# Kernel optimization log

Measured on AMD Instinct MI355X. Metric: run time of the kernel, lower is better.

Reference implementation:

```python
import jax, jax.numpy as jnp
import numpy as np

EPS = 1e-7
N_NODES = 30000
N_EDGES = 300000
GNN_DIM = 256
ENC_HID = 128
OUT_DIM = 3
N_LAYERS = 4


def _glorot(key, shape):
    fan_in, fan_out = shape[-2], shape[-1]
    s = jnp.sqrt(6.0 / (fan_in + fan_out))
    return jax.random.uniform(key, shape, jnp.float32, -s, s)


def setup_inputs() -> dict:
    key = jax.random.key(0)
    ks = jax.random.split(key, 12)
    x = jax.random.normal(ks[0], (N_NODES, 1), jnp.float32)
    edge_attr = jax.random.normal(ks[1], (N_EDGES, 1), jnp.float32)
    edge_index = jax.random.randint(ks[2], (2, N_EDGES), 0, N_NODES, jnp.int64)
    return {
        "x": x,
        "edge_attr": edge_attr,
        "edge_index": edge_index,
        # node encoder MLP: 1 -> 128 -> ReLU -> 256
        "node_w1": _glorot(ks[3], (1, ENC_HID)),
        "node_b1": jnp.zeros((ENC_HID,), jnp.float32),
        "node_w2": _glorot(ks[4], (ENC_HID, GNN_DIM)),
        "node_b2": jnp.zeros((GNN_DIM,), jnp.float32),
        # edge encoder MLP: 1 -> 128 -> ReLU -> 256
        "edge_w1": _glorot(ks[5], (1, ENC_HID)),
        "edge_b1": jnp.zeros((ENC_HID,), jnp.float32),
        "edge_w2": _glorot(ks[6], (ENC_HID, GNN_DIM)),
        "edge_b2": jnp.zeros((GNN_DIM,), jnp.float32),
        # 4 GENConv layers, each internal MLP is a single Linear(256, 256)
        "gnn_w": _glorot(ks[7], (N_LAYERS, GNN_DIM, GNN_DIM)),
        "gnn_b": jnp.zeros((N_LAYERS, GNN_DIM), jnp.float32),
        # output head: Linear(256, 3)
        "out_w": _glorot(ks[8], (GNN_DIM, OUT_DIM)),
        "out_b": jnp.zeros((OUT_DIM,), jnp.float32),
    }


def reference(x, edge_attr, edge_index, node_w1, node_b1, node_w2, node_b2,
              edge_w1, edge_b1, edge_w2, edge_b2, gnn_w, gnn_b, out_w, out_b):
    n = x.shape[0]
    # encoders (MLP, no norm, ReLU between layers, plain last layer)
    h = jax.nn.relu(x @ node_w1 + node_b1) @ node_w2 + node_b2            # [N, 256]
    e = jax.nn.relu(edge_attr @ edge_w1 + edge_b1) @ edge_w2 + edge_b2    # [E, 256]
    src = edge_index[0]  # x_j (source, messages flow source -> target)
    dst = edge_index[1]  # aggregation target
    for l in range(gnn_w.shape[0]):
        # GENConv message: relu(x_j + edge_attr) + eps
        msg = jax.nn.relu(h[src] + e) + EPS                               # [E, 256]
        agg = jax.ops.segment_sum(msg, dst, num_segments=n)               # [N, 256]
        # update: mlp(aggr + x_dst); num_layers=1 -> single Linear
        h = (agg + h) @ gnn_w[l] + gnn_b[l]
    return h @ out_w + out_b                                              # [N, 3]
```

## Files before the change

kernel.cpp:

```cpp
#include <hip/hip_runtime.h>
#include <stdint.h>

#define EPS_F 1e-7f

typedef float f32x4 __attribute__((ext_vector_type(4)));
typedef float f32x8 __attribute__((ext_vector_type(8)));
typedef short short8 __attribute__((ext_vector_type(8)));
typedef unsigned short u16;
typedef unsigned short ushort4v __attribute__((ext_vector_type(4)));
typedef unsigned short ushort8v __attribute__((ext_vector_type(8)));
typedef unsigned int uint4v __attribute__((ext_vector_type(4)));

__device__ __forceinline__ short f2bf(float f) {
  unsigned u = __float_as_uint(f);
  unsigned r = u + 0x7FFFu + ((u >> 16) & 1u);
  return (short)(r >> 16);
}
__device__ __forceinline__ float bf2f(u16 u) {
  return __uint_as_float((unsigned)u << 16);
}

__global__ void build_meta_kernel(const float* __restrict__ w1, const float* __restrict__ b1,
                                  float* __restrict__ knots, int* __restrict__ jrank,
                                  int* __restrict__ act0, int* __restrict__ segsel) {
  __shared__ float s_kx[128];
  __shared__ float s_sorted[128];
  int t = threadIdx.x;
  float w = w1[t], b = b1[t];
  float kx = (w != 0.0f) ? (-b / w) : 3.4e38f;
  s_kx[t] = kx;
  int a0 = (w < 0.0f) || (w == 0.0f && b > 0.0f);
  __syncthreads();
  int r = 0;
  for (int i = 0; i < 128; ++i) {
    float o = s_kx[i];
    if (o < kx || (o == kx && i < t)) ++r;
  }
  jrank[t] = r;
  act0[t] = a0;
  knots[r] = kx;
  s_sorted[r] = kx;
  __syncthreads();
  if (t == 0 && segsel) {
    int lo = 0, hi = 128;
    while (lo < hi) { int m = (lo + hi) >> 1; if (s_sorted[m] < -1.0f) lo = m + 1; else hi = m; }
    segsel[0] = lo;
    lo = 0; hi = 128;
    while (lo < hi) { int m = (lo + hi) >> 1; if (s_sorted[m] < 1.0f) lo = m + 1; else hi = m; }
    segsel[1] = lo;
  }
}

__global__ void build_seg_kernel(const float* __restrict__ w1, const float* __restrict__ b1,
                                 const float* __restrict__ w2, const float* __restrict__ b2,
                                 const int* __restrict__ jrank, const int* __restrict__ act0,
                                 float* __restrict__ segA, float* __restrict__ segB,
                                 unsigned* __restrict__ ABpack) {
  int s = blockIdx.x;
  int t = threadIdx.x;
  __shared__ float s_w1[128], s_b1[128];
  __shared__ int s_on[128];
  if (t < 128) {
    s_w1[t] = w1[t];
    s_b1[t] = b1[t];
    s_on[t] = act0[t] ^ (jrank[t] < s ? 1 : 0);
  }
  __syncthreads();
  float A = 0.0f, B = b2[t];
#pragma unroll 4
  for (int j = 0; j < 128; ++j) {
    if (s_on[j]) {
      float w2v = w2[j * 256 + t];
      A = fmaf(s_w1[j], w2v, A);
      B = fmaf(s_b1[j], w2v, B);
    }
  }
  segA[s * 256 + t] = A;
  segB[s * 256 + t] = B;
  if (ABpack) {
    unsigned a = (unsigned)(u16)f2bf(A);
    unsigned bb = (unsigned)(u16)f2bf(B);
    ABpack[s * 256 + t] = a | (bb << 16);
  }
}

__global__ void apply_enc_kernel(const float* __restrict__ in, int nrows,
                                 const float* __restrict__ knots, const float* __restrict__ segA,
                                 const float* __restrict__ segB, u16* __restrict__ outbf) {
  __shared__ float s_kx[128];
  int t = threadIdx.x;
  if (t < 128) s_kx[t] = knots[t];
  __syncthreads();
  int r0 = blockIdx.x * 16;
  int rEnd = r0 + 16;
  if (rEnd > nrows) rEnd = nrows;
  for (int r = r0; r < rEnd; ++r) {
    float x = in[r];
    int lo = 0, hi = 128;
    while (lo < hi) { int mid = (lo + hi) >> 1; if (s_kx[mid] < x) lo = mid + 1; else hi = mid; }
    outbf[(size_t)r * 256 + t] = (u16)f2bf(fmaf(segA[lo * 256 + t], x, segB[lo * 256 + t]));
  }
}

__global__ void zero_kernel(int* __restrict__ p, int n) {
  int i = blockIdx.x * blockDim.x + threadIdx.x;
  if (i < n) p[i] = 0;
}

__global__ void hist_kernel(const int* __restrict__ dst, int E, int* __restrict__ counts) {
  int i = blockIdx.x * blockDim.x + threadIdx.x;
  if (i < E) atomicAdd(&counts[dst[i]], 1);
}

__global__ void scan_p1_kernel(const int* __restrict__ counts, int n,
                               int* __restrict__ blocksums) {
  __shared__ int tmp[256];
  int t = threadIdx.x;
  int i = blockIdx.x * 256 + t;
  tmp[t] = (i < n) ? counts[i] : 0;
  __syncthreads();
  for (int off = 128; off > 0; off >>= 1) {
    if (t < off) tmp[t] += tmp[t + off];
    __syncthreads();
  }
  if (t == 0) blocksums[blockIdx.x] = tmp[0];
}

__global__ void scan_p2_kernel(int* __restrict__ blocksums, int nb,
                               int* __restrict__ row_start, int n) {
  __shared__ int tmp[256];
  int t = threadIdx.x;
  int v = (t < nb) ? blocksums[t] : 0;
  tmp[t] = v;
  __syncthreads();
  for (int off = 1; off < 256; off <<= 1) {
    int add = (t >= off) ? tmp[t - off] : 0;
    __syncthreads();
    tmp[t] += add;
    __syncthreads();
  }
  if (t < nb) blocksums[t] = tmp[t] - v;
  if (t == 0) row_start[n] = tmp[255];
}

__global__ void scan_p3_kernel(const int* __restrict__ counts, int n,
                               const int* __restrict__ blocksums,
                               int* __restrict__ row_start) {
  __shared__ int tmp[256];
  int t = threadIdx.x;
  int i = blockIdx.x * 256 + t;
  int v = (i < n) ? counts[i] : 0;
  tmp[t] = v;
  __syncthreads();
  for (int off = 1; off < 256; off <<= 1) {
    int add = (t >= off) ? tmp[t - off] : 0;
    __syncthreads();
    tmp[t] += add;
    __syncthreads();
  }
  if (i < n) row_start[i] = blocksums[blockIdx.x] + tmp[t] - v;
}

__global__ void fill_kernel(const int* __restrict__ srcA, const int* __restrict__ dstA,
                            const float* __restrict__ eattr, int E,
                            const int* __restrict__ row_start, int* __restrict__ cursor,
                            const float* __restrict__ knotsE, int2* __restrict__ csr) {
  __shared__ float s_kx[128];
  if (threadIdx.x < 128) s_kx[threadIdx.x] = knotsE[threadIdx.x];
  __syncthreads();
  int i = blockIdx.x * blockDim.x + threadIdx.x;
  if (i >= E) return;
  int s = srcA[i], d = dstA[i];
  float x = eattr[i];
  int lo = 0, hi = 128;
  while (lo < hi) { int mid = (lo + hi) >> 1; if (s_kx[mid] < x) lo = mid + 1; else hi = mid; }
  int pos = row_start[d] + atomicAdd(&cursor[d], 1);
  csr[pos] = make_int2(s | (lo << 17), __float_as_int(x));
}

__global__ void convw_kernel(const float* __restrict__ W, short* __restrict__ WT) {
  int l = blockIdx.x >> 8, nn = blockIdx.x & 255, k = threadIdx.x;
  WT[((size_t)l * 256 + nn) * 256 + k] = f2bf(W[((size_t)l * 256 + k) * 256 + nn]);
}

#define PAIR_FETCH(k)                                                              \
  int si##k = p + 2 * (k) + half; si##k = (si##k < hi) ? si##k : hi - 1;           \
  int2 e##k = ec[si##k];                                                           \
  ushort8v hv##k = *(const ushort8v*)(hbf + (size_t)(e##k.x & 0x1FFFF) * 256 + dl);

#define PAIR_COMP(k) {                                                             \
    float mk = (p + 2 * (k) + half < hi) ? 1.0f : 0.0f;                            \
    float xk = __int_as_float(e##k.y);                                             \
    int gk = e##k.x >> 17;                                                         \
    if (__builtin_expect(__ballot(gk != segN && gk != segP) != 0ull, 0)) {         \
      uint4v ab0 = *(const uint4v*)(AB + (size_t)gk * 256 + dl);                   \
      uint4v ab1 = *(const uint4v*)(AB + (size_t)gk * 256 + dl + 4);               \
      _Pragma("unroll") for (int j = 0; j < 8; ++j) {                              \
        unsigned abj = (j < 4) ? ab0[j] : ab1[j - 4];                              \
        float Ae = __uint_as_float(abj << 16);                                     \
        float Be = __uint_as_float(abj & 0xFFFF0000u);                             \
        float tt = bf2f(hv##k[j]) + fmaf(Ae, xk, Be);                              \
        acc[j] = fmaf(mk, fmaxf(tt, 0.0f), acc[j]);                                \
      }                                                                            \
    } else {                                                                       \
      bool isN = (gk == segN);                                                     \
      _Pragma("unroll") for (int j = 0; j < 8; ++j) {                              \
        float Ae = isN ? An[j] : Ap[j];                                            \
        float Be = isN ? Bn[j] : Bp[j];                                            \
        float tt = bf2f(hv##k[j]) + fmaf(Ae, xk, Be);                              \
        acc[j] = fmaf(mk, fmaxf(tt, 0.0f), acc[j]);                                \
      }                                                                            \
    }                                                                              \
  }

__global__ __launch_bounds__(256, 2) void layer_kernel(
    const u16* __restrict__ hbf, const int2* __restrict__ csr,
    const int* __restrict__ rowSt,
    const unsigned* __restrict__ AB, const int* __restrict__ segsel,
    const short* __restrict__ WT, const float* __restrict__ bias,
    u16* __restrict__ houtbf, float* __restrict__ outp,
    const float* __restrict__ ow3, const float* __restrict__ ob3, int N) {
  __shared__ u16 As[16][264];
  __shared__ int2 ecache[4][256];
  __shared__ float sw[768];
  __shared__ float sh[4][16][3];
  int wv = threadIdx.x >> 6, lane = threadIdx.x & 63;
  int nbase = blockIdx.x * 16;
  int d0 = lane * 4;
  int v0 = nbase + wv * 4;
  int half = lane >> 5;
  int dl = (lane & 31) * 8;

  if (outp) {
    for (int i = threadIdx.x; i < 768; i += 256) sw[i] = ow3[i];
  }

  int segN = segsel[0], segP = segsel[1];
  f32x8 An, Bn, Ap, Bp;
  {
    uint4v n0 = *(const uint4v*)(AB + (size_t)segN * 256 + dl);
    uint4v n1 = *(const uint4v*)(AB + (size_t)segN * 256 + dl + 4);
    uint4v p0v = *(const uint4v*)(AB + (size_t)segP * 256 + dl);
    uint4v p1v = *(const uint4v*)(AB + (size_t)segP * 256 + dl + 4);
#pragma unroll
    for (int j = 0; j < 8; ++j) {
      unsigned nj = (j < 4) ? n0[j] : n1[j - 4];
      unsigned pj = (j < 4) ? p0v[j] : p1v[j - 4];
      An[j] = __uint_as_float(nj << 16);
      Bn[j] = __uint_as_float(nj & 0xFFFF0000u);
      Ap[j] = __uint_as_float(pj << 16);
      Bp[j] = __uint_as_float(pj & 0xFFFF0000u);
    }
  }

  int rv0 = rowSt[v0], rv1 = rowSt[v0 + 1], rv2 = rowSt[v0 + 2];
  int rv3 = rowSt[v0 + 3], rv4 = rowSt[v0 + 4];
  int range = rv4 - rv0;
  const int2* ec = &ecache[wv][0];

  if (__builtin_expect(range <= 256, 1)) {
    for (int s = lane; s < range; s += 64) ecache[wv][s] = csr[(size_t)rv0 + s];
    for (int i = 0; i < 4; ++i) {
      int v = v0 + i;
      int lo = ((i == 0) ? rv0 : (i == 1) ? rv1 : (i == 2) ? rv2 : rv3) - rv0;
      int hi = ((i == 0) ? rv1 : (i == 1) ? rv2 : (i == 2) ? rv3 : rv4) - rv0;
      int deg = hi - lo;
      ushort8v sv = *(const ushort8v*)(hbf + (size_t)v * 256 + dl);
      float de = (float)deg * EPS_F;
      f32x8 acc = {0.f, 0.f, 0.f, 0.f, 0.f, 0.f, 0.f, 0.f};
      for (int p = lo; p < hi; p += 8) {
        PAIR_FETCH(0); PAIR_FETCH(1); PAIR_FETCH(2); PAIR_FETCH(3);
        PAIR_COMP(0); PAIR_COMP(1); PAIR_COMP(2); PAIR_COMP(3);
      }
      ushort8v ob;
#pragma unroll
      for (int j = 0; j < 8; ++j) {
        float tot = acc[j] + __shfl_xor(acc[j], 32);
        ob[j] = (u16)f2bf(bf2f(sv[j]) + de + tot);
      }
      if (half == 0) *(ushort8v*)&As[wv * 4 + i][dl] = ob;
    }
  } else {
    for (int i = 0; i < 4; ++i) {
      int v = v0 + i;
      int lo = (i == 0) ? rv0 : (i == 1) ? rv1 : (i == 2) ? rv2 : rv3;
      int hi = (i == 0) ? rv1 : (i == 1) ? rv2 : (i == 2) ? rv3 : rv4;
      int deg = hi - lo;
      ushort4v sv = *(const ushort4v*)(hbf + (size_t)v * 256 + d0);
      float de = (float)deg * EPS_F;
      f32x4 acc;
      acc.x = bf2f(sv.x) + de; acc.y = bf2f(sv.y) + de;
      acc.z = bf2f(sv.z) + de; acc.w = bf2f(sv.w) + de;
      for (int p = lo; p < hi; ++p) {
        int2 e = csr[(size_t)p];
        ushort4v hv = *(const ushort4v*)(hbf + (size_t)(e.x & 0x1FFFF) * 256 + d0);
        float x = __int_as_float(e.y);
        int g = __builtin_amdgcn_readfirstlane(e.x) >> 17;
        f32x4 Ae, Be;
        uint4v ab = *(const uint4v*)(AB + (size_t)g * 256 + d0);
#pragma unroll
        for (int j = 0; j < 4; ++j) {
          Ae[j] = __uint_as_float(ab[j] << 16);
          Be[j] = __uint_as_float(ab[j] & 0xFFFF0000u);
        }
#pragma unroll
        for (int j = 0; j < 4; ++j)
          acc[j] += fmaxf(bf2f(hv[j]) + fmaf(Ae[j], x, Be[j]), 0.0f);
      }
      ushort4v ob;
      ob.x = (u16)f2bf(acc.x); ob.y = (u16)f2bf(acc.y);
      ob.z = (u16)f2bf(acc.z); ob.w = (u16)f2bf(acc.w);
      *(ushort4v*)&As[wv * 4 + i][d0] = ob;
    }
  }
  __syncthreads();

  int colb = lane & 15, rowf = lane & 15, kgrp = (lane >> 4) * 8;
  int c0 = wv * 64;
  const short* wtc = WT + (size_t)(c0 + colb) * 256;
  const u16* Ar = &As[rowf][0];
  f32x4 acc0 = {0.f, 0.f, 0.f, 0.f}, acc1 = acc0, acc2 = acc0, acc3 = acc0;
  short8 b0 = *(const short8*)(wtc + kgrp);
  short8 b1 = *(const short8*)(wtc + 4096 + kgrp);
  short8 b2 = *(const short8*)(wtc + 8192 + kgrp);
  short8 b3 = *(const short8*)(wtc + 12288 + kgrp);
#pragma unroll
  for (int kt = 0; kt < 8; ++kt) {
    int k0 = kt * 32 + kgrp;
    short8 af = *(const short8*)(Ar + k0);
    short8 n0, n1, n2, n3;
    if (kt < 7) {
      int kn = k0 + 32;
      n0 = *(const short8*)(wtc + kn);
      n1 = *(const short8*)(wtc + 4096 + kn);
      n2 = *(const short8*)(wtc + 8192 + kn);
      n3 = *(const short8*)(wtc + 12288 + kn);
    }
    acc0 = __builtin_amdgcn_mfma_f32_16x16x32_bf16(af, b0, acc0, 0, 0, 0);
    acc1 = __builtin_amdgcn_mfma_f32_16x16x32_bf16(af, b1, acc1, 0, 0, 0);
    acc2 = __builtin_amdgcn_mfma_f32_16x16x32_bf16(af, b2, acc2, 0, 0, 0);
    acc3 = __builtin_amdgcn_mfma_f32_16x16x32_bf16(af, b3, acc3, 0, 0, 0);
    if (kt < 7) { b0 = n0; b1 = n1; b2 = n2; b3 = n3; }
  }
  int rbase = (lane >> 4) * 4;
  if (houtbf) {
#pragma unroll
    for (int nbk = 0; nbk < 4; ++nbk) {
      f32x4 a = (nbk == 0) ? acc0 : (nbk == 1) ? acc1 : (nbk == 2) ? acc2 : acc3;
      int col = c0 + nbk * 16 + colb;
      float bv = bias[col];
#pragma unroll
      for (int rr = 0; rr < 4; ++rr) {
        int vv = nbase + rbase + rr;
        if (vv < N) houtbf[(size_t)vv * 256 + col] = (u16)f2bf(a[rr] + bv);
      }
    }
  }
  if (outp) {
    float p[4][3];
#pragma unroll
    for (int rr = 0; rr < 4; ++rr) {
      p[rr][0] = 0.f; p[rr][1] = 0.f; p[rr][2] = 0.f;
    }
#pragma unroll
    for (int nbk = 0; nbk < 4; ++nbk) {
      f32x4 a = (nbk == 0) ? acc0 : (nbk == 1) ? acc1 : (nbk == 2) ? acc2 : acc3;
      int col = c0 + nbk * 16 + colb;
      float bv = bias[col];
#pragma unroll
      for (int rr = 0; rr < 4; ++rr) {
        float val = a[rr] + bv;
#pragma unroll
        for (int o = 0; o < 3; ++o) p[rr][o] = fmaf(val, sw[col * 3 + o], p[rr][o]);
      }
    }
#pragma unroll
    for (int rr = 0; rr < 4; ++rr)
#pragma unroll
      for (int o = 0; o < 3; ++o) {
        float s = p[rr][o];
        s += __shfl_xor(s, 1, 16);
        s += __shfl_xor(s, 2, 16);
        s += __shfl_xor(s, 4, 16);
        s += __shfl_xor(s, 8, 16);
        if (colb == 0) sh[wv][rbase + rr][o] = s;
      }
    __syncthreads();
    int t = threadIdx.x;
    if (t < 48) {
      int row = t / 3, o = t % 3;
      float s = sh[0][row][o] + sh[1][row][o] + sh[2][row][o] + sh[3][row][o] + ob3[o];
      int vv = nbase + row;
      if (vv < N) outp[(size_t)vv * 3 + o] = s;
    }
  }
}

extern "C" void kernel_launch(void* const* d_in, const int* in_sizes, int n_in,
                              void* d_out, int out_size, void* d_ws, size_t ws_size,
                              hipStream_t stream) {
  const float* x     = (const float*)d_in[0];
  const float* eattr = (const float*)d_in[1];
  const int*   eidx  = (const int*)d_in[2];
  const float* nw1 = (const float*)d_in[3];
  const float* nb1 = (const float*)d_in[4];
  const float* nw2 = (const float*)d_in[5];
  const float* nb2 = (const float*)d_in[6];
  const float* ew1 = (const float*)d_in[7];
  const float* eb1 = (const float*)d_in[8];
  const float* ew2 = (const float*)d_in[9];
  const float* eb2 = (const float*)d_in[10];
  const float* gw  = (const float*)d_in[11];
  const float* gb  = (const float*)d_in[12];
  const float* ow  = (const float*)d_in[13];
  const float* ob  = (const float*)d_in[14];

  int N = in_sizes[0];
  int E = in_sizes[1];
  const int* srcA = eidx;
  const int* dstA = eidx + E;

  char* ws = (char*)d_ws;
  auto al = [](size_t v) { return (v + 255) & ~(size_t)255; };
  size_t off = 0;
  u16* hbfA    = (u16*)(ws + off);   off = al(off + (size_t)N * 256 * 2);
  u16* hbfB    = (u16*)(ws + off);   off = al(off + (size_t)N * 256 * 2);
  short* WT    = (short*)(ws + off); off = al(off + (size_t)4 * 256 * 256 * 2);
  float* knN   = (float*)(ws + off); off = al(off + 128 * 4);
  float* AN    = (float*)(ws + off); off = al(off + 129 * 256 * 4);
  float* BN    = (float*)(ws + off); off = al(off + 129 * 256 * 4);
  float* knE   = (float*)(ws + off); off = al(off + 128 * 4);
  float* AE    = (float*)(ws + off); off = al(off + 129 * 256 * 4);
  float* BE    = (float*)(ws + off); off = al(off + 129 * 256 * 4);
  unsigned* ABE = (unsigned*)(ws + off); off = al(off + 129 * 256 * 4);
  int* rankN   = (int*)(ws + off);   off = al(off + 128 * 4);
  int* act0N   = (int*)(ws + off);   off = al(off + 128 * 4);
  int* rankE   = (int*)(ws + off);   off = al(off + 128 * 4);
  int* act0E   = (int*)(ws + off);   off = al(off + 128 * 4);
  int* segselE = (int*)(ws + off);   off = al(off + 2 * 4);
  int* rowSt   = (int*)(ws + off);   off = al(off + (size_t)(N + 1) * 4);
  int* counts  = (int*)(ws + off);   off = al(off + (size_t)N * 4);
  int* bsums   = (int*)(ws + off);   off = al(off + 256 * 4);
  int2* csr    = (int2*)(ws + off);  off = al(off + (size_t)E * 8);
  (void)ws_size; (void)n_in; (void)out_size;

  build_meta_kernel<<<1, 128, 0, stream>>>(nw1, nb1, knN, rankN, act0N, nullptr);
  build_meta_kernel<<<1, 128, 0, stream>>>(ew1, eb1, knE, rankE, act0E, segselE);
  build_seg_kernel<<<129, 256, 0, stream>>>(nw1, nb1, nw2, nb2, rankN, act0N, AN, BN, nullptr);
  build_seg_kernel<<<129, 256, 0, stream>>>(ew1, eb1, ew2, eb2, rankE, act0E, AE, BE, ABE);

  apply_enc_kernel<<<(N + 15) / 16, 256, 0, stream>>>(x, N, knN, AN, BN, hbfA);

  int gN = (N + 255) / 256, gE = (E + 255) / 256;
  zero_kernel<<<gN, 256, 0, stream>>>(counts, N);
  hist_kernel<<<gE, 256, 0, stream>>>(dstA, E, counts);
  scan_p1_kernel<<<gN, 256, 0, stream>>>(counts, N, bsums);
  scan_p2_kernel<<<1, 256, 0, stream>>>(bsums, gN, rowSt, N);
  scan_p3_kernel<<<gN, 256, 0, stream>>>(counts, N, bsums, rowSt);
  zero_kernel<<<gN, 256, 0, stream>>>(counts, N);
  fill_kernel<<<gE, 256, 0, stream>>>(srcA, dstA, eattr, E, rowSt, counts, knE, csr);

  convw_kernel<<<4 * 256, 256, 0, stream>>>(gw, WT);

  u16* hbc = hbfA;
  u16* hbn = hbfB;
  int gLayer = (N + 15) / 16;
  for (int l = 0; l < 4; ++l) {
    u16* hbo = (l == 3) ? nullptr : hbn;
    float* op = (l == 3) ? (float*)d_out : nullptr;
    layer_kernel<<<gLayer, 256, 0, stream>>>(hbc, csr, rowSt, ABE, segselE,
                                             WT + (size_t)l * 256 * 256,
                                             gb + (size_t)l * 256, hbo, op, ow, ob, N);
    u16* t = hbc; hbc = hbn; hbn = t;
  }
}
```

Before: 353.4 us.

## Merge setup kernels and widen layer blocks to eight waves of two nodes

Merges the node and edge encoder setup kernels into single launches, and folds the node encoding, count zeroing and weight conversion into one fused launch. This cuts the number of small kernel launches. The layer kernel now runs 512 threads per block, with each wave aggregating 2 nodes instead of 4 and computing 32 output columns instead of 64. The aim is more waves in flight to hide gather latency, at the cost of a smaller per-wave edge cache, so high-degree node pairs hit the slow path more often, plus more block-level sync overhead.

```diff
diff --git a/kernel.cpp b/kernel.cpp
--- a/kernel.cpp
+++ b/kernel.cpp
@@ -20,11 +20,20 @@
   return __uint_as_float((unsigned)u << 16);
 }
 
-__global__ void build_meta_kernel(const float* __restrict__ w1, const float* __restrict__ b1,
-                                  float* __restrict__ knots, int* __restrict__ jrank,
-                                  int* __restrict__ act0, int* __restrict__ segsel) {
+__global__ void build_meta2_kernel(const float* __restrict__ nw1, const float* __restrict__ nb1,
+                                   const float* __restrict__ ew1, const float* __restrict__ eb1,
+                                   float* __restrict__ knN, int* __restrict__ rankN,
+                                   int* __restrict__ act0N,
+                                   float* __restrict__ knE, int* __restrict__ rankE,
+                                   int* __restrict__ act0E, int* __restrict__ segsel) {
   __shared__ float s_kx[128];
   __shared__ float s_sorted[128];
+  int isE = blockIdx.x;
+  const float* w1 = isE ? ew1 : nw1;
+  const float* b1 = isE ? eb1 : nb1;
+  float* knots = isE ? knE : knN;
+  int* jrank = isE ? rankE : rankN;
+  int* act0 = isE ? act0E : act0N;
   int t = threadIdx.x;
   float w = w1[t], b = b1[t];
   float kx = (w != 0.0f) ? (-b / w) : 3.4e38f;
@@ -41,7 +50,7 @@
   knots[r] = kx;
   s_sorted[r] = kx;
   __syncthreads();
-  if (t == 0 && segsel) {
+  if (t == 0 && isE) {
     int lo = 0, hi = 128;
     while (lo < hi) { int m = (lo + hi) >> 1; if (s_sorted[m] < -1.0f) lo = m + 1; else hi = m; }
     segsel[0] = lo;
@@ -51,13 +60,23 @@
   }
 }
 
-__global__ void build_seg_kernel(const float* __restrict__ w1, const float* __restrict__ b1,
-                                 const float* __restrict__ w2, const float* __restrict__ b2,
-                                 const int* __restrict__ jrank, const int* __restrict__ act0,
-                                 float* __restrict__ segA, float* __restrict__ segB,
-                                 unsigned* __restrict__ ABpack) {
-  int s = blockIdx.x;
-  int t = threadIdx.x;
+__global__ void build_seg2_kernel(const float* __restrict__ nw1, const float* __restrict__ nb1,
+                                  const float* __restrict__ nw2, const float* __restrict__ nb2,
+                                  const float* __restrict__ ew1, const float* __restrict__ eb1,
+                                  const float* __restrict__ ew2, const float* __restrict__ eb2,
+                                  const int* __restrict__ rankN, const int* __restrict__ act0N,
+                                  const int* __restrict__ rankE, const int* __restrict__ act0E,
+                                  float* __restrict__ AN, float* __restrict__ BN,
+                                  unsigned* __restrict__ ABE) {
+  int isE = (blockIdx.x >= 129);
+  int s = isE ? (blockIdx.x - 129) : blockIdx.x;
+  int t = threadIdx.x;
+  const float* w1 = isE ? ew1 : nw1;
+  const float* b1 = isE ? eb1 : nb1;
+  const float* w2 = isE ? ew2 : nw2;
+  const float* b2 = isE ? eb2 : nb2;
+  const int* jrank = isE ? rankE : rankN;
+  const int* act0 = isE ? act0E : act0N;
   __shared__ float s_w1[128], s_b1[128];
   __shared__ int s_on[128];
   if (t < 128) {
@@ -75,36 +94,44 @@
       B = fmaf(s_b1[j], w2v, B);
     }
   }
-  segA[s * 256 + t] = A;
-  segB[s * 256 + t] = B;
-  if (ABpack) {
+  if (!isE) {
+    AN[s * 256 + t] = A;
+    BN[s * 256 + t] = B;
+  } else {
     unsigned a = (unsigned)(u16)f2bf(A);
     unsigned bb = (unsigned)(u16)f2bf(B);
-    ABpack[s * 256 + t] = a | (bb << 16);
-  }
-}
-
-__global__ void apply_enc_kernel(const float* __restrict__ in, int nrows,
+    ABE[s * 256 + t] = a | (bb << 16);
+  }
+}
+
+__global__ void enc_fused_kernel(const float* __restrict__ in, int nrows, int gEnc, int gZero,
                                  const float* __restrict__ knots, const float* __restrict__ segA,
-                                 const float* __restrict__ segB, u16* __restrict__ outbf) {
-  __shared__ float s_kx[128];
-  int t = threadIdx.x;
-  if (t < 128) s_kx[t] = knots[t];
-  __syncthreads();
-  int r0 = blockIdx.x * 16;
-  int rEnd = r0 + 16;
-  if (rEnd > nrows) rEnd = nrows;
-  for (int r = r0; r < rEnd; ++r) {
-    float x = in[r];
-    int lo = 0, hi = 128;
-    while (lo < hi) { int mid = (lo + hi) >> 1; if (s_kx[mid] < x) lo = mid + 1; else hi = mid; }
-    outbf[(size_t)r * 256 + t] = (u16)f2bf(fmaf(segA[lo * 256 + t], x, segB[lo * 256 + t]));
-  }
-}
-
-__global__ void zero_kernel(int* __restrict__ p, int n) {
-  int i = blockIdx.x * blockDim.x + threadIdx.x;
-  if (i < n) p[i] = 0;
+                                 const float* __restrict__ segB, u16* __restrict__ outbf,
+                                 int* __restrict__ counts,
+                                 const float* __restrict__ W, short* __restrict__ WT) {
+  int bid = blockIdx.x;
+  int t = threadIdx.x;
+  if (bid < gEnc) {
+    __shared__ float s_kx[128];
+    if (t < 128) s_kx[t] = knots[t];
+    __syncthreads();
+    int r0 = bid * 16;
+    int rEnd = r0 + 16;
+    if (rEnd > nrows) rEnd = nrows;
+    for (int r = r0; r < rEnd; ++r) {
+      float x = in[r];
+      int lo = 0, hi = 128;
+      while (lo < hi) { int mid = (lo + hi) >> 1; if (s_kx[mid] < x) lo = mid + 1; else hi = mid; }
+      outbf[(size_t)r * 256 + t] = (u16)f2bf(fmaf(segA[lo * 256 + t], x, segB[lo * 256 + t]));
+    }
+  } else if (bid < gEnc + gZero) {
+    int i = (bid - gEnc) * 256 + t;
+    if (i < nrows) counts[i] = 0;
+  } else {
+    int cb = bid - gEnc - gZero;
+    int l = cb >> 8, nn = cb & 255, k = t;
+    WT[((size_t)l * 256 + nn) * 256 + k] = f2bf(W[((size_t)l * 256 + k) * 256 + nn]);
+  }
 }
 
 __global__ void hist_kernel(const int* __restrict__ dst, int E, int* __restrict__ counts) {
@@ -159,6 +186,11 @@
     __syncthreads();
   }
   if (i < n) row_start[i] = blocksums[blockIdx.x] + tmp[t] - v;
+}
+
+__global__ void zero_kernel(int* __restrict__ p, int n) {
+  int i = blockIdx.x * blockDim.x + threadIdx.x;
+  if (i < n) p[i] = 0;
 }
 
 __global__ void fill_kernel(const int* __restrict__ srcA, const int* __restrict__ dstA,
@@ -176,11 +208,6 @@
   while (lo < hi) { int mid = (lo + hi) >> 1; if (s_kx[mid] < x) lo = mid + 1; else hi = mid; }
   int pos = row_start[d] + atomicAdd(&cursor[d], 1);
   csr[pos] = make_int2(s | (lo << 17), __float_as_int(x));
-}
-
-__global__ void convw_kernel(const float* __restrict__ W, short* __restrict__ WT) {
-  int l = blockIdx.x >> 8, nn = blockIdx.x & 255, k = threadIdx.x;
-  WT[((size_t)l * 256 + nn) * 256 + k] = f2bf(W[((size_t)l * 256 + k) * 256 + nn]);
 }
 
 #define PAIR_FETCH(k)                                                              \
@@ -213,7 +240,7 @@
     }                                                                              \
   }
 
-__global__ __launch_bounds__(256, 2) void layer_kernel(
+__global__ __launch_bounds__(512, 6) void layer_kernel(
     const u16* __restrict__ hbf, const int2* __restrict__ csr,
     const int* __restrict__ rowSt,
     const unsigned* __restrict__ AB, const int* __restrict__ segsel,
@@ -221,18 +248,18 @@
     u16* __restrict__ houtbf, float* __restrict__ outp,
     const float* __restrict__ ow3, const float* __restrict__ ob3, int N) {
   __shared__ u16 As[16][264];
-  __shared__ int2 ecache[4][256];
+  __shared__ int2 ecache[8][128];
   __shared__ float sw[768];
-  __shared__ float sh[4][16][3];
+  __shared__ float sh[8][16][3];
   int wv = threadIdx.x >> 6, lane = threadIdx.x & 63;
   int nbase = blockIdx.x * 16;
   int d0 = lane * 4;
-  int v0 = nbase + wv * 4;
+  int v0 = nbase + wv * 2;
   int half = lane >> 5;
   int dl = (lane & 31) * 8;
 
   if (outp) {
-    for (int i = threadIdx.x; i < 768; i += 256) sw[i] = ow3[i];
+    for (int i = threadIdx.x; i < 768; i += 512) sw[i] = ow3[i];
   }
 
   int segN = segsel[0], segP = segsel[1];
@@ -254,16 +281,15 @@
   }
 
   int rv0 = rowSt[v0], rv1 = rowSt[v0 + 1], rv2 = rowSt[v0 + 2];
-  int rv3 = rowSt[v0 + 3], rv4 = rowSt[v0 + 4];
-  int range = rv4 - rv0;
+  int range = rv2 - rv0;
   const int2* ec = &ecache[wv][0];
 
-  if (__builtin_expect(range <= 256, 1)) {
+  if (__builtin_expect(range <= 128, 1)) {
     for (int s = lane; s < range; s += 64) ecache[wv][s] = csr[(size_t)rv0 + s];
-    for (int i = 0; i < 4; ++i) {
+    for (int i = 0; i < 2; ++i) {
       int v = v0 + i;
-      int lo = ((i == 0) ? rv0 : (i == 1) ? rv1 : (i == 2) ? rv2 : rv3) - rv0;
-      int hi = ((i == 0) ? rv1 : (i == 1) ? rv2 : (i == 2) ? rv3 : rv4) - rv0;
+      int lo = ((i == 0) ? rv0 : rv1) - rv0;
+      int hi = ((i == 0) ? rv1 : rv2) - rv0;
       int deg = hi - lo;
       ushort8v sv = *(const ushort8v*)(hbf + (size_t)v * 256 + dl);
       float de = (float)deg * EPS_F;
@@ -278,13 +304,13 @@
         float tot = acc[j] + __shfl_xor(acc[j], 32);
         ob[j] = (u16)f2bf(bf2f(sv[j]) + de + tot);
       }
-      if (half == 0) *(ushort8v*)&As[wv * 4 + i][dl] = ob;
+      if (half == 0) *(ushort8v*)&As[wv * 2 + i][dl] = ob;
     }
   } else {
-    for (int i = 0; i < 4; ++i) {
+    for (int i = 0; i < 2; ++i) {
       int v = v0 + i;
-      int lo = (i == 0) ? rv0 : (i == 1) ? rv1 : (i == 2) ? rv2 : rv3;
-      int hi = (i == 0) ? rv1 : (i == 1) ? rv2 : (i == 2) ? rv3 : rv4;
+      int lo = (i == 0) ? rv0 : rv1;
+      int hi = (i == 0) ? rv1 : rv2;
       int deg = hi - lo;
       ushort4v sv = *(const ushort4v*)(hbf + (size_t)v * 256 + d0);
       float de = (float)deg * EPS_F;
@@ -310,43 +336,37 @@
       ushort4v ob;
       ob.x = (u16)f2bf(acc.x); ob.y = (u16)f2bf(acc.y);
       ob.z = (u16)f2bf(acc.z); ob.w = (u16)f2bf(acc.w);
-      *(ushort4v*)&As[wv * 4 + i][d0] = ob;
+      *(ushort4v*)&As[wv * 2 + i][d0] = ob;
     }
   }
   __syncthreads();
 
   int colb = lane & 15, rowf = lane & 15, kgrp = (lane >> 4) * 8;
-  int c0 = wv * 64;
+  int c0 = wv * 32;
   const short* wtc = WT + (size_t)(c0 + colb) * 256;
   const u16* Ar = &As[rowf][0];
-  f32x4 acc0 = {0.f, 0.f, 0.f, 0.f}, acc1 = acc0, acc2 = acc0, acc3 = acc0;
+  f32x4 acc0 = {0.f, 0.f, 0.f, 0.f}, acc1 = acc0;
   short8 b0 = *(const short8*)(wtc + kgrp);
   short8 b1 = *(const short8*)(wtc + 4096 + kgrp);
-  short8 b2 = *(const short8*)(wtc + 8192 + kgrp);
-  short8 b3 = *(const short8*)(wtc + 12288 + kgrp);
 #pragma unroll
   for (int kt = 0; kt < 8; ++kt) {
     int k0 = kt * 32 + kgrp;
     short8 af = *(const short8*)(Ar + k0);
-    short8 n0, n1, n2, n3;
+    short8 n0, n1;
     if (kt < 7) {
       int kn = k0 + 32;
       n0 = *(const short8*)(wtc + kn);
       n1 = *(const short8*)(wtc + 4096 + kn);
-      n2 = *(const short8*)(wtc + 8192 + kn);
-      n3 = *(const short8*)(wtc + 12288 + kn);
     }
     acc0 = __builtin_amdgcn_mfma_f32_16x16x32_bf16(af, b0, acc0, 0, 0, 0);
     acc1 = __builtin_amdgcn_mfma_f32_16x16x32_bf16(af, b1, acc1, 0, 0, 0);
-    acc2 = __builtin_amdgcn_mfma_f32_16x16x32_bf16(af, b2, acc2, 0, 0, 0);
-    acc3 = __builtin_amdgcn_mfma_f32_16x16x32_bf16(af, b3, acc3, 0, 0, 0);
-    if (kt < 7) { b0 = n0; b1 = n1; b2 = n2; b3 = n3; }
+    if (kt < 7) { b0 = n0; b1 = n1; }
   }
   int rbase = (lane >> 4) * 4;
   if (houtbf) {
 #pragma unroll
-    for (int nbk = 0; nbk < 4; ++nbk) {
-      f32x4 a = (nbk == 0) ? acc0 : (nbk == 1) ? acc1 : (nbk == 2) ? acc2 : acc3;
+    for (int nbk = 0; nbk < 2; ++nbk) {
+      f32x4 a = (nbk == 0) ? acc0 : acc1;
       int col = c0 + nbk * 16 + colb;
       float bv = bias[col];
 #pragma unroll
@@ -363,8 +383,8 @@
       p[rr][0] = 0.f; p[rr][1] = 0.f; p[rr][2] = 0.f;
     }
 #pragma unroll
-    for (int nbk = 0; nbk < 4; ++nbk) {
-      f32x4 a = (nbk == 0) ? acc0 : (nbk == 1) ? acc1 : (nbk == 2) ? acc2 : acc3;
+    for (int nbk = 0; nbk < 2; ++nbk) {
+      f32x4 a = (nbk == 0) ? acc0 : acc1;
       int col = c0 + nbk * 16 + colb;
       float bv = bias[col];
 #pragma unroll
@@ -389,7 +409,9 @@
     int t = threadIdx.x;
     if (t < 48) {
       int row = t / 3, o = t % 3;
-      float s = sh[0][row][o] + sh[1][row][o] + sh[2][row][o] + sh[3][row][o] + ob3[o];
+      float s = ob3[o];
+#pragma unroll
+      for (int w = 0; w < 8; ++w) s += sh[w][row][o];
       int vv = nbase + row;
       if (vv < N) outp[(size_t)vv * 3 + o] = s;
     }
@@ -430,8 +452,6 @@
   float* AN    = (float*)(ws + off); off = al(off + 129 * 256 * 4);
   float* BN    = (float*)(ws + off); off = al(off + 129 * 256 * 4);
   float* knE   = (float*)(ws + off); off = al(off + 128 * 4);
-  float* AE    = (float*)(ws + off); off = al(off + 129 * 256 * 4);
-  float* BE    = (float*)(ws + off); off = al(off + 129 * 256 * 4);
   unsigned* ABE = (unsigned*)(ws + off); off = al(off + 129 * 256 * 4);
   int* rankN   = (int*)(ws + off);   off = al(off + 128 * 4);
   int* act0N   = (int*)(ws + off);   off = al(off + 128 * 4);
@@ -444,15 +464,17 @@
   int2* csr    = (int2*)(ws + off);  off = al(off + (size_t)E * 8);
   (void)ws_size; (void)n_in; (void)out_size;
 
-  build_meta_kernel<<<1, 128, 0, stream>>>(nw1, nb1, knN, rankN, act0N, nullptr);
-  build_meta_kernel<<<1, 128, 0, stream>>>(ew1, eb1, knE, rankE, act0E, segselE);
-  build_seg_kernel<<<129, 256, 0, stream>>>(nw1, nb1, nw2, nb2, rankN, act0N, AN, BN, nullptr);
-  build_seg_kernel<<<129, 256, 0, stream>>>(ew1, eb1, ew2, eb2, rankE, act0E, AE, BE, ABE);
-
-  apply_enc_kernel<<<(N + 15) / 16, 256, 0, stream>>>(x, N, knN, AN, BN, hbfA);
-
   int gN = (N + 255) / 256, gE = (E + 255) / 256;
-  zero_kernel<<<gN, 256, 0, stream>>>(counts, N);
+  int gEnc = (N + 15) / 16;
+
+  build_meta2_kernel<<<2, 128, 0, stream>>>(nw1, nb1, ew1, eb1, knN, rankN, act0N,
+                                            knE, rankE, act0E, segselE);
+  build_seg2_kernel<<<258, 256, 0, stream>>>(nw1, nb1, nw2, nb2, ew1, eb1, ew2, eb2,
+                                             rankN, act0N, rankE, act0E, AN, BN, ABE);
+
+  enc_fused_kernel<<<gEnc + gN + 1024, 256, 0, stream>>>(x, N, gEnc, gN, knN, AN, BN,
+                                                         hbfA, counts, gw, WT);
+
   hist_kernel<<<gE, 256, 0, stream>>>(dstA, E, counts);
   scan_p1_kernel<<<gN, 256, 0, stream>>>(counts, N, bsums);
   scan_p2_kernel<<<1, 256, 0, stream>>>(bsums, gN, rowSt, N);
@@ -460,15 +482,13 @@
   zero_kernel<<<gN, 256, 0, stream>>>(counts, N);
   fill_kernel<<<gE, 256, 0, stream>>>(srcA, dstA, eattr, E, rowSt, counts, knE, csr);
 
-  convw_kernel<<<4 * 256, 256, 0, stream>>>(gw, WT);
-
   u16* hbc = hbfA;
   u16* hbn = hbfB;
   int gLayer = (N + 15) / 16;
   for (int l = 0; l < 4; ++l) {
     u16* hbo = (l == 3) ? nullptr : hbn;
     float* op = (l == 3) ? (float*)d_out : nullptr;
-    layer_kernel<<<gLayer, 256, 0, stream>>>(hbc, csr, rowSt, ABE, segselE,
+    layer_kernel<<<gLayer, 512, 0, stream>>>(hbc, csr, rowSt, ABE, segselE,
                                              WT + (size_t)l * 256 * 256,
                                              gb + (size_t)l * 256, hbo, op, ow, ob, N);
     u16* t = hbc; hbc = hbn; hbn = t;
```

Result: slower. 574.2 us (+62.5%).
